# Performance work log

Hardware: AMD Instinct MI355X
Metric: run time of the kernel (lower is better)

Reference implementation:

```python
import jax, jax.numpy as jnp
import numpy as np

# --- static CT geometry (shapes must be static under jit; mirrors the `options` vector) ---
B = 8          # batch
V = 720        # number of projection views
D = 736        # detector bins per view
H = 512        # image height (pixels)
W = 512        # image width  (pixels)
DIMG = 0.006641            # image pixel size (physical units)
DDET = 0.0066              # detector bin size
ANG0 = 0.0                 # starting angle
DANG = 2.0 * np.pi / V     # angular step


def setup_inputs() -> dict:
    key = jax.random.key(0)
    proj = jax.random.normal(key, (B, 1, V, D), dtype=jnp.float32)
    options = jnp.array(
        [V, D, W, H, DIMG, DDET, ANG0, DANG, 5.95, 4.906, 0.0, 2.0],
        dtype=jnp.float32,
    )
    return {"proj": proj, "options": options}


def _backproject(sino):
    """Pixel-driven parallel-beam back-projection of one sinogram [V, D] -> image [H, W]."""
    xs = (jnp.arange(W, dtype=jnp.float32) - (W - 1) / 2.0) * DIMG   # pixel-center x
    ys = ((H - 1) / 2.0 - jnp.arange(H, dtype=jnp.float32)) * DIMG   # pixel-center y
    x = jnp.broadcast_to(xs[None, :], (H, W))
    y = jnp.broadcast_to(ys[:, None], (H, W))
    angles = ANG0 + jnp.arange(V, dtype=jnp.float32) * DANG

    def body(acc, inp):
        ang, row = inp                               # row: [D] detector samples at this view
        t = x * jnp.cos(ang) + y * jnp.sin(ang)      # ray coordinate of each pixel
        u = t / DDET + (D - 1) / 2.0                 # fractional detector index
        u0 = jnp.floor(u)
        w = u - u0
        i0 = u0.astype(jnp.int32)
        i1 = i0 + 1
        v0 = jnp.where((i0 >= 0) & (i0 < D), row[jnp.clip(i0, 0, D - 1)], 0.0)
        v1 = jnp.where((i1 >= 0) & (i1 < D), row[jnp.clip(i1, 0, D - 1)], 0.0)
        return acc + (1.0 - w) * v0 + w * v1, None

    acc, _ = jax.lax.scan(body, jnp.zeros((H, W), jnp.float32), (angles, sino))
    return acc * DANG  # angular integration weight


def reference(proj, options):
    # `options` carries the geometry; its shape-determining entries are baked in statically.
    sino = proj.reshape(B, V, D)
    img = jax.vmap(_backproject)(sino)
    return img.reshape(B, 1, H, W)
```

## Files before the change

### kernel.cpp

```cpp
#include <hip/hip_runtime.h>

#define BATCH 8
#define NVIEW 720
#define NPAIR 360
#define NGRP  180
#define NDET  736
#define IMGH  512
#define IMGW  512

#define DANG_F  ((float)(6.283185307179586 / 720.0))
#define RATIO_F ((float)(0.006641 / 0.0066))
#define UCENTER ((float)((NDET - 1) * 0.5))

#define PADDET 768
#define ITER_BYTES 12288
#define WS_BYTES ((size_t)BATCH * NGRP * 2 * PADDET * 4)

typedef float  v2f __attribute__((ext_vector_type(2)));
typedef __fp16 v2h __attribute__((ext_vector_type(2)));

__global__ __launch_bounds__(192) void prep_kernel(
    const float* __restrict__ proj, v2h* __restrict__ ws)
{
    const int t = threadIdx.x;
    if (t >= 184) return;
    const int y = blockIdx.x;
    const int b = blockIdx.y;
    const int g    = y >> 1;
    const int pair = y & 1;
    const int frow = g + 180 * pair;
    const int i = 4 * t;
    const float* __restrict__ fwd = proj + ((size_t)b * NVIEW + frow) * NDET;
    const float* __restrict__ rev = fwd + (size_t)NPAIR * NDET;
    const float4 f4 = *(const float4*)(fwd + i);
    const float  f1 = fwd[i + 4];
    const float4 r4 = *(const float4*)(rev + (732 - i));
    const float  r1 = rev[731 - i];
    const float s0 = f4.x + r4.w;
    const float s1 = f4.y + r4.z;
    const float s2 = f4.z + r4.y;
    const float s3 = f4.w + r4.x;
    const float s4 = f1 + r1;
    const v2h n0 = __builtin_amdgcn_cvt_pkrtz(s1 - s0, s0);
    const v2h n1 = __builtin_amdgcn_cvt_pkrtz(s2 - s1, s1);
    const v2h n2 = __builtin_amdgcn_cvt_pkrtz(s3 - s2, s2);
    const v2h n3 = __builtin_amdgcn_cvt_pkrtz(s4 - s3, s3);
    struct alignas(16) H4 { v2h a, b, c, d; };
    *(H4*)(ws + ((size_t)b * NGRP * 2 + y) * PADDET + i) = H4{n0, n1, n2, n3};
}

__device__ __forceinline__ void visit(const v2h* __restrict__ L,
                                      float u, float& accA, float& accB) {
    const int   i0 = (int)u;
    const float fr = __builtin_amdgcn_fractf(u);
    const v2h wv = __builtin_amdgcn_cvt_pkrtz(fr, 1.0f);
    const v2h A = L[i0];
    const v2h B = L[i0 + PADDET];
    accA = __builtin_amdgcn_fdot2(A, wv, accA, false);
    accB = __builtin_amdgcn_fdot2(B, wv, accB, false);
}

__global__ __launch_bounds__(512, 4) void backproject_dma_kernel(
    const v2h* __restrict__ ws, float* __restrict__ out)
{
    __shared__ alignas(16) v2h lds4[4][2 * 2 * PADDET];
    __shared__ v2f cs[NGRP];

    const int tid  = threadIdx.x;
    const int wave = tid >> 6;
    const int lane = tid & 63;

    if (tid < NGRP) {
        float s, c;
        sincosf((float)tid * DANG_F, &s, &c);
        cs[tid] = (v2f){c * RATIO_F, s * RATIO_F};
    }

    const int b  = blockIdx.z;
    const int h  = (int)blockIdx.y * 8 + wave;
    const int w0 = (int)blockIdx.x * 64 + lane;

    const float px = (float)w0 - (float)(IMGW - 1) * 0.5f;
    const float py = (float)(IMGH - 1) * 0.5f - (float)h;

    const char* __restrict__ wsb =
        (const char*)(ws + (size_t)b * NGRP * 2 * PADDET);

    float a0 = 0.f, a1 = 0.f, a2 = 0.f, a3 = 0.f;
    float b0 = 0.f, b1 = 0.f, b2 = 0.f, b3 = 0.f;

    auto issue = [&](int p) {
        const char* g0 = wsb + (size_t)p * ITER_BYTES;
        char* l0 = (char*)&lds4[p & 3][0];
        __builtin_amdgcn_global_load_lds(
            (const __attribute__((address_space(1))) void*)
                (g0 + wave * 1024 + lane * 16),
            (__attribute__((address_space(3))) void*)(l0 + wave * 1024),
            16, 0, 0);
        if (wave < 4) {
            const int s = 8 + wave;
            __builtin_amdgcn_global_load_lds(
                (const __attribute__((address_space(1))) void*)
                    (g0 + s * 1024 + lane * 16),
                (__attribute__((address_space(3))) void*)(l0 + s * 1024),
                16, 0, 0);
        }
    };

    auto groups = [&](int p) {
        const v2h* __restrict__ L4 = &lds4[p & 3][0];
#pragma unroll
        for (int sub = 0; sub < 2; ++sub) {
            const v2h* __restrict__ L = L4 + sub * (2 * PADDET);
            const v2f t = cs[2 * p + sub];
            const v2f m1 = {t.x, -t.y};
            const v2f m2 = {t.y, t.x};
            const v2f pxv = {px, px};
            const v2f pyv = {py, py};
            const v2f gvec = __builtin_elementwise_fma(pxv, m1, pyv * m2);
            const v2f cc = {UCENTER, UCENTER};
            const v2f up = cc + gvec;
            const v2f um = cc - gvec;
            const v2f dd = {128.0f, 128.0f};
            const v2f dm = dd * m1;
            const v2f vp = up + dm;
            const v2f vm = um - dm;

            visit(L, up.x, a0, a1);
            visit(L, um.x, a2, a3);
            visit(L, up.y, a3, a0);
            visit(L, um.y, a1, a2);
            visit(L, vp.x, b0, b1);
            visit(L, vm.x, b2, b3);
            visit(L, vp.y, b3, b0);
            visit(L, vm.y, b1, b2);
        }
    };

    issue(0);
    __syncthreads();
    for (int p = 0; p < 90; ++p) {
        if (p + 1 < 90) issue(p + 1);
        groups(p);
        if (p + 1 < 90) __syncthreads();
    }

    float* __restrict__ o = out + (size_t)b * IMGH * IMGW;
    const int hm  = (IMGH - 1) - h;
    const int w1  = w0 + 128;
    const int wm0 = (IMGW - 1) - w0;
    const int wm1 = (IMGW - 1) - w1;
    o[h   * IMGW + w0 ] = a0 * DANG_F;
    o[wm0 * IMGW + h  ] = a1 * DANG_F;
    o[hm  * IMGW + wm0] = a2 * DANG_F;
    o[w0  * IMGW + hm ] = a3 * DANG_F;
    o[h   * IMGW + w1 ] = b0 * DANG_F;
    o[wm1 * IMGW + h  ] = b1 * DANG_F;
    o[hm  * IMGW + wm1] = b2 * DANG_F;
    o[w1  * IMGW + hm ] = b3 * DANG_F;
}

struct Stage { float4 f4, r4; float f1, r1; };

__device__ __forceinline__ void fb_load(const float* __restrict__ sino,
                                        int k, int t, Stage& S) {
    if (t < 368) {
        const int p  = (t >= 184);
        const int i  = 4 * (t - 184 * p);
        const int vf = k + 180 * p;
        const float* __restrict__ fwd = sino + vf * NDET;
        const float* __restrict__ rev = sino + (vf + NPAIR) * NDET;
        S.f4 = *(const float4*)(fwd + i);
        S.f1 = fwd[i + 4];
        S.r4 = *(const float4*)(rev + (732 - i));
        S.r1 = rev[731 - i];
    }
}

__device__ __forceinline__ void fb_write(v2h* __restrict__ L, int t,
                                         const Stage& S) {
    if (t < 368) {
        const int p = (t >= 184);
        const int i = 4 * (t - 184 * p);
        const float s0 = S.f4.x + S.r4.w;
        const float s1 = S.f4.y + S.r4.z;
        const float s2 = S.f4.z + S.r4.y;
        const float s3 = S.f4.w + S.r4.x;
        const float s4 = S.f1 + S.r1;
        const v2h n0 = __builtin_amdgcn_cvt_pkrtz(s1 - s0, s0);
        const v2h n1 = __builtin_amdgcn_cvt_pkrtz(s2 - s1, s1);
        const v2h n2 = __builtin_amdgcn_cvt_pkrtz(s3 - s2, s2);
        const v2h n3 = __builtin_amdgcn_cvt_pkrtz(s4 - s3, s3);
        struct alignas(16) H4 { v2h a, b, c, d; };
        *(H4*)(L + p * NDET + i) = H4{n0, n1, n2, n3};
    }
}

__device__ __forceinline__ void fb_visit(const v2h* __restrict__ L,
                                         float u, float& accA, float& accB) {
    const int   i0 = (int)u;
    const float fr = __builtin_amdgcn_fractf(u);
    const v2h wv = __builtin_amdgcn_cvt_pkrtz(fr, 1.0f);
    const v2h A = L[i0];
    const v2h B = L[i0 + NDET];
    accA = __builtin_amdgcn_fdot2(A, wv, accA, false);
    accB = __builtin_amdgcn_fdot2(B, wv, accB, false);
}

__global__ __launch_bounds__(512, 4) void backproject_fb_kernel(
    const float* __restrict__ proj, float* __restrict__ out)
{
    __shared__ alignas(16) v2h lds[2][2][2 * NDET];
    __shared__ v2f cs[NGRP];

    const int tid = threadIdx.x;
    if (tid < NGRP) {
        float s, c;
        sincosf((float)tid * DANG_F, &s, &c);
        cs[tid] = (v2f){c * RATIO_F, s * RATIO_F};
    }

    const int b    = blockIdx.z;
    const int lane = tid & 63;
    const int h    = (int)blockIdx.y * 8 + (tid >> 6);
    const int w0   = (int)blockIdx.x * 64 + lane;

    const float px = (float)w0 - (float)(IMGW - 1) * 0.5f;
    const float py = (float)(IMGH - 1) * 0.5f - (float)h;

    const float* __restrict__ sino = proj + (size_t)b * NVIEW * NDET;

    float a0 = 0.f, a1 = 0.f, a2 = 0.f, a3 = 0.f;
    float b0 = 0.f, b1 = 0.f, b2 = 0.f, b3 = 0.f;

    Stage s0 = {}, s1 = {};
    fb_load(sino, 0, tid, s0);
    fb_load(sino, 1, tid, s1);
    fb_write(lds[0][0], tid, s0);
    fb_write(lds[0][1], tid, s1);
    fb_load(sino, 2, tid, s0);
    fb_load(sino, 3, tid, s1);
    __syncthreads();

    for (int gg = 0; gg < NGRP; gg += 2) {
        const int buf = (gg >> 1) & 1;
#pragma unroll
        for (int sub = 0; sub < 2; ++sub) {
            const v2h* __restrict__ L = lds[buf][sub];
            const v2f t = cs[gg + sub];
            const v2f m1 = {t.x, -t.y};
            const v2f m2 = {t.y, t.x};
            const v2f pxv = {px, px};
            const v2f pyv = {py, py};
            const v2f gvec = __builtin_elementwise_fma(pxv, m1, pyv * m2);
            const v2f cc = {UCENTER, UCENTER};
            const v2f up = cc + gvec;
            const v2f um = cc - gvec;
            const v2f dd = {128.0f, 128.0f};
            const v2f dm = dd * m1;
            const v2f vp = up + dm;
            const v2f vm = um - dm;

            fb_visit(L, up.x, a0, a1);
            fb_visit(L, um.x, a2, a3);
            fb_visit(L, up.y, a3, a0);
            fb_visit(L, um.y, a1, a2);
            fb_visit(L, vp.x, b0, b1);
            fb_visit(L, vm.x, b2, b3);
            fb_visit(L, vp.y, b3, b0);
            fb_visit(L, vm.y, b1, b2);
        }
        if (gg < NGRP - 2) {
            fb_write(lds[buf ^ 1][0], tid, s0);
            fb_write(lds[buf ^ 1][1], tid, s1);
            if (gg < NGRP - 4) {
                fb_load(sino, gg + 4, tid, s0);
                fb_load(sino, gg + 5, tid, s1);
            }
            __syncthreads();
        }
    }

    float* __restrict__ o = out + (size_t)b * IMGH * IMGW;
    const int hm  = (IMGH - 1) - h;
    const int w1  = w0 + 128;
    const int wm0 = (IMGW - 1) - w0;
    const int wm1 = (IMGW - 1) - w1;
    o[h   * IMGW + w0 ] = a0 * DANG_F;
    o[wm0 * IMGW + h  ] = a1 * DANG_F;
    o[hm  * IMGW + wm0] = a2 * DANG_F;
    o[w0  * IMGW + hm ] = a3 * DANG_F;
    o[h   * IMGW + w1 ] = b0 * DANG_F;
    o[wm1 * IMGW + h  ] = b1 * DANG_F;
    o[hm  * IMGW + wm1] = b2 * DANG_F;
    o[w1  * IMGW + hm ] = b3 * DANG_F;
}

extern "C" void kernel_launch(void* const* d_in, const int* in_sizes, int n_in,
                              void* d_out, int out_size, void* d_ws, size_t ws_size,
                              hipStream_t stream) {
    const float* proj = (const float*)d_in[0];
    float* out = (float*)d_out;

    if (ws_size >= WS_BYTES) {
        v2h* ws = (v2h*)d_ws;
        prep_kernel<<<dim3(360, BATCH), 192, 0, stream>>>(proj, ws);
        backproject_dma_kernel<<<dim3(2, 32, BATCH), 512, 0, stream>>>(ws, out);
    } else {
        backproject_fb_kernel<<<dim3(2, 32, BATCH), 512, 0, stream>>>(proj, out);
    }
}
```

Before: 169.1 us.

## Exploit diagonal mirror symmetry and pack four view planes into 16-byte entries

Adds the diagonal reflection on top of the existing four-fold rotational symmetry, so each thread now handles a pixel in one triangular octant plus its mirror, with special handling for the diagonal and for the 0/45-degree views. The prep kernel now interleaves four paired view planes (g, g+180, mirror m, m+180) into one 16-byte entry per detector bin. A single 128-bit LDS read can then feed four fdot2 accumulations instead of two 32-bit reads feeding two. This is meant to halve LDS read instructions per accumulation. In exchange it adds divergent branches for diagonal pixels and more complex index and store logic.

```diff
diff --git a/kernel.cpp b/kernel.cpp
--- a/kernel.cpp
+++ b/kernel.cpp
@@ -13,57 +13,96 @@
 #define UCENTER ((float)((NDET - 1) * 0.5))
 
 #define PADDET 768
+#define NITER  90
 #define ITER_BYTES 12288
-#define WS_BYTES ((size_t)BATCH * NGRP * 2 * PADDET * 4)
+#define WS_BYTES ((size_t)BATCH * NITER * PADDET * 16)
 
 typedef float  v2f __attribute__((ext_vector_type(2)));
 typedef __fp16 v2h __attribute__((ext_vector_type(2)));
-
-__global__ __launch_bounds__(192) void prep_kernel(
-    const float* __restrict__ proj, v2h* __restrict__ ws)
-{
-    const int t = threadIdx.x;
-    if (t >= 184) return;
-    const int y = blockIdx.x;
-    const int b = blockIdx.y;
-    const int g    = y >> 1;
-    const int pair = y & 1;
-    const int frow = g + 180 * pair;
-    const int i = 4 * t;
-    const float* __restrict__ fwd = proj + ((size_t)b * NVIEW + frow) * NDET;
-    const float* __restrict__ rev = fwd + (size_t)NPAIR * NDET;
+typedef __fp16 v8h __attribute__((ext_vector_type(8)));
+
+struct alignas(16) E16 { v2h ag, bg, am, bm; };
+
+__device__ __forceinline__ void fuse5(const float* __restrict__ fwd,
+                                      const float* __restrict__ rev,
+                                      int i, float s[5]) {
     const float4 f4 = *(const float4*)(fwd + i);
     const float  f1 = fwd[i + 4];
     const float4 r4 = *(const float4*)(rev + (732 - i));
     const float  r1 = rev[731 - i];
-    const float s0 = f4.x + r4.w;
-    const float s1 = f4.y + r4.z;
-    const float s2 = f4.z + r4.y;
-    const float s3 = f4.w + r4.x;
-    const float s4 = f1 + r1;
-    const v2h n0 = __builtin_amdgcn_cvt_pkrtz(s1 - s0, s0);
-    const v2h n1 = __builtin_amdgcn_cvt_pkrtz(s2 - s1, s1);
-    const v2h n2 = __builtin_amdgcn_cvt_pkrtz(s3 - s2, s2);
-    const v2h n3 = __builtin_amdgcn_cvt_pkrtz(s4 - s3, s3);
-    struct alignas(16) H4 { v2h a, b, c, d; };
-    *(H4*)(ws + ((size_t)b * NGRP * 2 + y) * PADDET + i) = H4{n0, n1, n2, n3};
-}
-
-__device__ __forceinline__ void visit(const v2h* __restrict__ L,
-                                      float u, float& accA, float& accB) {
-    const int   i0 = (int)u;
-    const float fr = __builtin_amdgcn_fractf(u);
-    const v2h wv = __builtin_amdgcn_cvt_pkrtz(fr, 1.0f);
-    const v2h A = L[i0];
-    const v2h B = L[i0 + PADDET];
-    accA = __builtin_amdgcn_fdot2(A, wv, accA, false);
-    accB = __builtin_amdgcn_fdot2(B, wv, accB, false);
-}
+    s[0] = f4.x + r4.w; s[1] = f4.y + r4.z; s[2] = f4.z + r4.y;
+    s[3] = f4.w + r4.x; s[4] = f1 + r1;
+}
+
+__global__ __launch_bounds__(192) void prep_kernel(
+    const float* __restrict__ proj, E16* __restrict__ ws)
+{
+    const int t = threadIdx.x;
+    if (t >= 184) return;
+    const int p = blockIdx.x;
+    const int b = blockIdx.y;
+    const int g = (p < 89) ? p + 1   : 0;
+    const int m = (p < 89) ? 179 - p : 90;
+    const int i = 4 * t;
+    const float* __restrict__ base = proj + (size_t)b * NVIEW * NDET;
+    float sAg[5], sBg[5], sAm[5], sBm[5];
+    fuse5(base + (size_t)g * NDET,         base + (size_t)(g + 360) * NDET, i, sAg);
+    fuse5(base + (size_t)(g + 180) * NDET, base + (size_t)(g + 540) * NDET, i, sBg);
+    fuse5(base + (size_t)m * NDET,         base + (size_t)(m + 360) * NDET, i, sAm);
+    fuse5(base + (size_t)(m + 180) * NDET, base + (size_t)(m + 540) * NDET, i, sBm);
+    E16* __restrict__ dst = ws + ((size_t)b * NITER + p) * PADDET + i;
+#pragma unroll
+    for (int k = 0; k < 4; ++k) {
+        E16 e;
+        e.ag = __builtin_amdgcn_cvt_pkrtz(sAg[k + 1] - sAg[k], sAg[k]);
+        e.bg = __builtin_amdgcn_cvt_pkrtz(sBg[k + 1] - sBg[k], sBg[k]);
+        e.am = __builtin_amdgcn_cvt_pkrtz(sAm[k + 1] - sAm[k], sAm[k]);
+        e.bm = __builtin_amdgcn_cvt_pkrtz(sBm[k + 1] - sBm[k], sBm[k]);
+        dst[k] = e;
+    }
+}
+
+#define VIS(Lp, u, r0, r1, r2, r3) do {                                      \
+    const float uu_ = (u);                                                   \
+    const int   ii_ = (int)uu_;                                              \
+    const v2h wv_ = __builtin_amdgcn_cvt_pkrtz(                              \
+        __builtin_amdgcn_fractf(uu_), 1.0f);                                 \
+    const v8h E_ = (Lp)[ii_];                                                \
+    r0 = __builtin_amdgcn_fdot2((v2h){E_[0], E_[1]}, wv_, r0, false);        \
+    r1 = __builtin_amdgcn_fdot2((v2h){E_[2], E_[3]}, wv_, r1, false);        \
+    r2 = __builtin_amdgcn_fdot2((v2h){E_[4], E_[5]}, wv_, r2, false);        \
+    r3 = __builtin_amdgcn_fdot2((v2h){E_[6], E_[7]}, wv_, r3, false);        \
+} while (0)
+
+#define VIS2(Lp, O, u, p0, p1, q0, q1) do {                                  \
+    const float uu_ = (u);                                                   \
+    const int   ii_ = (int)uu_;                                              \
+    const v2h wv_ = __builtin_amdgcn_cvt_pkrtz(                              \
+        __builtin_amdgcn_fractf(uu_), 1.0f);                                 \
+    const v8h E_ = (Lp)[ii_];                                                \
+    const v2h ha_ = {E_[(O)], E_[(O) + 1]};                                  \
+    const v2h hb_ = {E_[(O) + 2], E_[(O) + 3]};                              \
+    p0 = __builtin_amdgcn_fdot2(ha_, wv_, p0, false);                        \
+    p1 = __builtin_amdgcn_fdot2(ha_, wv_, p1, false);                        \
+    q0 = __builtin_amdgcn_fdot2(hb_, wv_, q0, false);                        \
+    q1 = __builtin_amdgcn_fdot2(hb_, wv_, q1, false);                        \
+} while (0)
+
+#define VIS1(Lp, O, u, p0, q0) do {                                          \
+    const float uu_ = (u);                                                   \
+    const int   ii_ = (int)uu_;                                              \
+    const v2h wv_ = __builtin_amdgcn_cvt_pkrtz(                              \
+        __builtin_amdgcn_fractf(uu_), 1.0f);                                 \
+    const v8h E_ = (Lp)[ii_];                                                \
+    p0 = __builtin_amdgcn_fdot2((v2h){E_[(O)], E_[(O) + 1]}, wv_, p0, false);\
+    q0 = __builtin_amdgcn_fdot2((v2h){E_[(O) + 2], E_[(O) + 3]}, wv_, q0,    \
+                                false);                                      \
+} while (0)
 
 __global__ __launch_bounds__(512, 4) void backproject_dma_kernel(
-    const v2h* __restrict__ ws, float* __restrict__ out)
+    const v8h* __restrict__ ws, float* __restrict__ out)
 {
-    __shared__ alignas(16) v2h lds4[4][2 * 2 * PADDET];
+    __shared__ alignas(16) v8h lds4[4][PADDET];
     __shared__ v2f cs[NGRP];
 
     const int tid  = threadIdx.x;
@@ -76,18 +115,27 @@
         cs[tid] = (v2f){c * RATIO_F, s * RATIO_F};
     }
 
-    const int b  = blockIdx.z;
-    const int h  = (int)blockIdx.y * 8 + wave;
-    const int w0 = (int)blockIdx.x * 64 + lane;
-
-    const float px = (float)w0 - (float)(IMGW - 1) * 0.5f;
-    const float py = (float)(IMGH - 1) * 0.5f - (float)h;
+    const int b = blockIdx.z;
+    const int h = (int)blockIdx.y * 8 + wave;
+    const int w = (int)blockIdx.x * 64 + lane;
+
+    const bool dg = (w == h);
+    const bool rm = (w > h);
+    const int  H  = rm ? 255 - h : h;
+    const int  W  = rm ? 255 - w : w;
+
+    const float px  = (float)W - 255.5f;
+    const float py  = 255.5f - (float)H;
+    const float px2 = dg ? (-0.5f - (float)W) : py;
+    const float py2 = dg ? ( 0.5f + (float)H) : px;
 
     const char* __restrict__ wsb =
-        (const char*)(ws + (size_t)b * NGRP * 2 * PADDET);
-
-    float a0 = 0.f, a1 = 0.f, a2 = 0.f, a3 = 0.f;
-    float b0 = 0.f, b1 = 0.f, b2 = 0.f, b3 = 0.f;
+        (const char*)(ws + (size_t)b * NITER * PADDET);
+
+    float A0 = 0.f, A1 = 0.f, A2 = 0.f, A3 = 0.f;
+    float B0 = 0.f, B1 = 0.f, B2 = 0.f, B3 = 0.f;
+    float X0 = 0.f, X1 = 0.f, X2 = 0.f, X3 = 0.f;
+    float Y0 = 0.f, Y1 = 0.f, Y2 = 0.f, Y3 = 0.f;
 
     auto issue = [&](int p) {
         const char* g0 = wsb + (size_t)p * ITER_BYTES;
@@ -107,57 +155,101 @@
         }
     };
 
-    auto groups = [&](int p) {
-        const v2h* __restrict__ L4 = &lds4[p & 3][0];
-#pragma unroll
-        for (int sub = 0; sub < 2; ++sub) {
-            const v2h* __restrict__ L = L4 + sub * (2 * PADDET);
-            const v2f t = cs[2 * p + sub];
+    issue(0);
+    __syncthreads();
+
+    const v2f cc = {UCENTER, UCENTER};
+    for (int p = 0; p < NITER - 1; ++p) {
+        issue(p + 1);
+        {
+            const v8h* __restrict__ L = &lds4[p & 3][0];
+            const v2f t  = cs[p + 1];
             const v2f m1 = {t.x, -t.y};
             const v2f m2 = {t.y, t.x};
-            const v2f pxv = {px, px};
-            const v2f pyv = {py, py};
-            const v2f gvec = __builtin_elementwise_fma(pxv, m1, pyv * m2);
-            const v2f cc = {UCENTER, UCENTER};
-            const v2f up = cc + gvec;
-            const v2f um = cc - gvec;
-            const v2f dd = {128.0f, 128.0f};
-            const v2f dm = dd * m1;
-            const v2f vp = up + dm;
-            const v2f vm = um - dm;
-
-            visit(L, up.x, a0, a1);
-            visit(L, um.x, a2, a3);
-            visit(L, up.y, a3, a0);
-            visit(L, um.y, a1, a2);
-            visit(L, vp.x, b0, b1);
-            visit(L, vm.x, b2, b3);
-            visit(L, vp.y, b3, b0);
-            visit(L, vm.y, b1, b2);
+            const v2f gA = __builtin_elementwise_fma(
+                (v2f){px, px}, m1, (v2f){py, py} * m2);
+            const v2f gB = __builtin_elementwise_fma(
+                (v2f){px2, px2}, m1, (v2f){py2, py2} * m2);
+            const v2f upA = cc + gA, umA = cc - gA;
+            const v2f upB = cc + gB, umB = cc - gB;
+            VIS(L, upA.x, A0, A1, X2, X3);
+            VIS(L, umA.x, A2, A3, X0, X1);
+            VIS(L, upA.y, A3, A0, X3, X0);
+            VIS(L, umA.y, A1, A2, X1, X2);
+            VIS(L, upB.x, B2, B3, Y0, Y1);
+            VIS(L, umB.x, B0, B1, Y2, Y3);
+            VIS(L, upB.y, B1, B2, Y1, Y2);
+            VIS(L, umB.y, B3, B0, Y3, Y0);
         }
-    };
-
-    issue(0);
-    __syncthreads();
-    for (int p = 0; p < 90; ++p) {
-        if (p + 1 < 90) issue(p + 1);
-        groups(p);
-        if (p + 1 < 90) __syncthreads();
-    }
+        __syncthreads();
+    }
+
+    {
+        const v8h* __restrict__ L = &lds4[(NITER - 1) & 3][0];
+        const v2f t0 = cs[0], t45 = cs[90];
+        if (!dg) {
+            const float g1 = px * t0.x + py * t0.y;
+            const float g2 = -px * t0.y + py * t0.x;
+            VIS2(L, 0, UCENTER + g1, A0, X1, A1, X2);
+            VIS2(L, 0, UCENTER - g1, A2, X3, A3, X0);
+            VIS2(L, 0, UCENTER + g2, A3, X2, A0, X3);
+            VIS2(L, 0, UCENTER - g2, A1, X0, A2, X1);
+            const float h1 = px * t45.x + py * t45.y;
+            const float h2 = -px * t45.y + py * t45.x;
+            VIS2(L, 4, UCENTER + h1, A0, X2, A1, X3);
+            VIS2(L, 4, UCENTER - h1, A2, X0, A3, X1);
+            VIS2(L, 4, UCENTER + h2, A3, X3, A0, X0);
+            VIS2(L, 4, UCENTER - h2, A1, X1, A2, X2);
+        } else {
+            const float g1  = px * t0.x + py * t0.y;
+            const float g1b = px2 * t0.x + py2 * t0.y;
+            VIS2(L, 0, UCENTER + g1,  A0, A1, A1, A2);
+            VIS2(L, 0, UCENTER - g1,  A2, A3, A0, A3);
+            VIS2(L, 0, UCENTER + g1b, B2, B3, B3, B0);
+            VIS2(L, 0, UCENTER - g1b, B0, B1, B2, B1);
+            {
+                const v2h wv_ = __builtin_amdgcn_cvt_pkrtz(0.5f, 1.0f);
+                const v8h E_ = L[(int)UCENTER];
+                const v2h ha_ = {E_[4], E_[5]};
+                const v2h hb_ = {E_[6], E_[7]};
+                A0 = __builtin_amdgcn_fdot2(ha_, wv_, A0, false);
+                A2 = __builtin_amdgcn_fdot2(ha_, wv_, A2, false);
+                B2 = __builtin_amdgcn_fdot2(ha_, wv_, B2, false);
+                B0 = __builtin_amdgcn_fdot2(ha_, wv_, B0, false);
+                A1 = __builtin_amdgcn_fdot2(hb_, wv_, A1, false);
+                A3 = __builtin_amdgcn_fdot2(hb_, wv_, A3, false);
+                B3 = __builtin_amdgcn_fdot2(hb_, wv_, B3, false);
+                B1 = __builtin_amdgcn_fdot2(hb_, wv_, B1, false);
+            }
+            const float e1 = (px + px) * t45.x;
+            const float e2 = (px2 + px2) * t45.x;
+            VIS1(L, 4, UCENTER + e1, A1, A2);
+            VIS1(L, 4, UCENTER - e1, A3, A0);
+            VIS1(L, 4, UCENTER + e2, B3, B0);
+            VIS1(L, 4, UCENTER - e2, B1, B2);
+        }
+    }
+
+    const float aE0 = dg ? X0 : Y0, aE1 = dg ? X1 : Y1;
+    const float aE2 = dg ? X2 : Y2, aE3 = dg ? X3 : Y3;
+    const float bE0 = dg ? Y0 : X0, bE1 = dg ? Y1 : X1;
+    const float bE2 = dg ? Y2 : X2, bE3 = dg ? Y3 : X3;
+    const float a0 = (A0 + aE0) * DANG_F, a1 = (A1 + aE1) * DANG_F;
+    const float a2 = (A2 + aE2) * DANG_F, a3 = (A3 + aE3) * DANG_F;
+    const float b0 = (B0 + bE0) * DANG_F, b1 = (B1 + bE1) * DANG_F;
+    const float b2 = (B2 + bE2) * DANG_F, b3 = (B3 + bE3) * DANG_F;
 
     float* __restrict__ o = out + (size_t)b * IMGH * IMGW;
-    const int hm  = (IMGH - 1) - h;
-    const int w1  = w0 + 128;
-    const int wm0 = (IMGW - 1) - w0;
-    const int wm1 = (IMGW - 1) - w1;
-    o[h   * IMGW + w0 ] = a0 * DANG_F;
-    o[wm0 * IMGW + h  ] = a1 * DANG_F;
-    o[hm  * IMGW + wm0] = a2 * DANG_F;
-    o[w0  * IMGW + hm ] = a3 * DANG_F;
-    o[h   * IMGW + w1 ] = b0 * DANG_F;
-    o[wm1 * IMGW + h  ] = b1 * DANG_F;
-    o[hm  * IMGW + wm1] = b2 * DANG_F;
-    o[w1  * IMGW + hm ] = b3 * DANG_F;
+    const int Qr = dg ? 256 + H : W;
+    const int Qc = dg ? 256 + W : H;
+    o[H * IMGW + W]                         = a0;
+    o[(511 - W) * IMGW + H]                 = a1;
+    o[(511 - H) * IMGW + (511 - W)]         = a2;
+    o[W * IMGW + (511 - H)]                 = a3;
+    o[Qr * IMGW + Qc]                       = b0;
+    o[(511 - Qc) * IMGW + Qr]               = b1;
+    o[(511 - Qr) * IMGW + (511 - Qc)]       = b2;
+    o[Qc * IMGW + (511 - Qr)]               = b3;
 }
 
 struct Stage { float4 f4, r4; float f1, r1; };
@@ -303,9 +395,10 @@
     float* out = (float*)d_out;
 
     if (ws_size >= WS_BYTES) {
-        v2h* ws = (v2h*)d_ws;
-        prep_kernel<<<dim3(360, BATCH), 192, 0, stream>>>(proj, ws);
-        backproject_dma_kernel<<<dim3(2, 32, BATCH), 512, 0, stream>>>(ws, out);
+        E16* ws = (E16*)d_ws;
+        prep_kernel<<<dim3(NITER, BATCH), 192, 0, stream>>>(proj, ws);
+        backproject_dma_kernel<<<dim3(2, 32, BATCH), 512, 0, stream>>>(
+            (const v8h*)ws, out);
     } else {
         backproject_fb_kernel<<<dim3(2, 32, BATCH), 512, 0, stream>>>(proj, out);
     }
```

New measurement: 144.7 us. -14.4%, faster.
